# Optimization experiments

Measured on AMD Instinct MI355X. Metric: run time of the kernel, lower is better.

## Reference

```python
import jax, jax.numpy as jnp
import numpy as np

D_STATE = 16


def setup_inputs() -> dict:
    key = jax.random.key(0)
    ks = jax.random.split(key, 7)
    B, S, D = 8, 4096, 64
    ds = D_STATE
    x = jax.random.normal(ks[0], (B, S, D), dtype=jnp.float32)
    # Selection layers modeled as Linear(d_model, out). W_A scaled small so the
    # random transition matrices are contractive over 4096 steps.
    W_A = jax.random.normal(ks[1], (D, ds * ds), dtype=jnp.float32) * 0.01
    b_A = jnp.zeros((ds * ds,), dtype=jnp.float32)
    W_B = jax.random.normal(ks[2], (D, ds * D), dtype=jnp.float32) * 0.05
    b_B = jnp.zeros((ds * D,), dtype=jnp.float32)
    W_C = jax.random.normal(ks[3], (D, ds * D), dtype=jnp.float32) * 0.05
    b_C = jnp.zeros((ds * D,), dtype=jnp.float32)
    return {"x": x, "W_A": W_A, "b_A": b_A, "W_B": W_B, "b_B": b_B,
            "W_C": W_C, "b_C": b_C}


def reference(x, W_A, b_A, W_B, b_B, W_C, b_C):
    B, S, D = x.shape
    ds = D_STATE
    # Input-dependent (selective) parameters per timestep
    A = (x @ W_A + b_A).reshape(B, S, ds, ds)      # [B,S,ds,ds]
    Bm = (x @ W_B + b_B).reshape(B, S, ds, D)      # [B,S,ds,D]
    Cm = (x @ W_C + b_C).reshape(B, S, ds, D)      # [B,S,ds,D]
    # Pre-contract B_t @ x_t once: [B,S,ds]
    Bx = jnp.einsum('bsnd,bsd->bsn', Bm, x)

    def step(h, inputs):
        A_t, Bx_t = inputs                          # [B,ds,ds], [B,ds]
        h = jnp.einsum('bij,bj->bi', A_t, h) + Bx_t
        return h, h

    h0 = jnp.zeros((B, ds), dtype=x.dtype)
    _, hs = jax.lax.scan(step, h0,
                         (jnp.swapaxes(A, 0, 1), jnp.swapaxes(Bx, 0, 1)))
    hs = jnp.swapaxes(hs, 0, 1)                     # [B,S,ds]
    # output_t = C_t^T @ h_t  -> [B,S,D]
    return jnp.einsum('bsnd,bsn->bsd', Cm, hs)
```

## Files before the change

kernel.cpp:

```cpp
#include <hip/hip_runtime.h>

#define BATCH   8
#define SEQ     4096
#define DM      64
#define DS      16
#define BS      (BATCH*SEQ)
#define CHUNK   16
#define NCHT    (BS/CHUNK)
#define SG      16
#define NSG     (NCHT/SG)

typedef __attribute__((ext_vector_type(8))) __bf16 bf16x8;
typedef __attribute__((ext_vector_type(4))) float  f32x4;

__device__ __forceinline__ unsigned short f2bf(float f) {
  unsigned int u = __float_as_uint(f);
  u += 0x7fffu + ((u >> 16) & 1u);
  return (unsigned short)(u >> 16);
}
__device__ __forceinline__ float bflo(unsigned int u) { return __uint_as_float(u << 16); }
__device__ __forceinline__ float bfhi(unsigned int u) { return __uint_as_float(u & 0xffff0000u); }

#define AS_I 20
#define AS_T 324

__global__ __launch_bounds__(256) void k0_castw(
    const float* __restrict__ WA, const float* __restrict__ WB,
    const float* __restrict__ WC,
    unsigned short* __restrict__ WBApk, unsigned short* __restrict__ WCpk)
{
  const int o = blockIdx.x * 256 + threadIdx.x;
  if (o < 81920) {
    int idx = o;
    const int e = idx & 7;    idx >>= 3;
    const int f = idx % 10;   idx /= 10;
    const int quad = idx & 3; idx >>= 2;
    const int l15 = idx & 15; idx >>= 4;
    const int n = idx;
    float src;
    if (f < 8) {
      const int r = f >> 1, h = f & 1;
      src = WB[(h * 32 + quad * 8 + e) * 1024 + (n * 4 + r) * 16 + l15];
    } else {
      const int h = f - 8;
      src = WA[(h * 32 + quad * 8 + e) * 256 + n * 16 + l15];
    }
    WBApk[o] = f2bf(src);
  } else {
    const int p = o - 81920;
    const int e = p & 7;
    const int h = (p >> 3) & 1;
    const int quad = (p >> 4) & 3;
    const int l15 = (p >> 6) & 15;
    const int nr = p >> 10;
    WCpk[p] = f2bf(WC[(h * 32 + quad * 8 + e) * 1024 + nr * 16 + l15]);
  }
}

struct WFrag {
  bf16x8 b00, b01, b10, b11, b20, b21, b30, b31;
  bf16x8 a0f, a1f;
  float  ba;
};

__device__ __forceinline__ WFrag loadw(
    const unsigned short* __restrict__ WBApk,
    const float* __restrict__ bA, int n, int l15, int quad)
{
  WFrag f;
  const bf16x8* fp = (const bf16x8*)(WBApk + (size_t)((n * 16 + l15) * 4 + quad) * 80);
  f.b00 = fp[0]; f.b01 = fp[1];
  f.b10 = fp[2]; f.b11 = fp[3];
  f.b20 = fp[4]; f.b21 = fp[5];
  f.b30 = fp[6]; f.b31 = fp[7];
  f.a0f = fp[8]; f.a1f = fp[9];
  f.ba  = bA[n * 16 + l15];
  return f;
}

__global__ __launch_bounds__(256, 2) void g1(
    const float* __restrict__ x, const unsigned short* __restrict__ WBApk,
    const float* __restrict__ bB,
    const float* __restrict__ bA, unsigned short* __restrict__ xb,
    unsigned short* __restrict__ Wt_ws, float* __restrict__ u_ws,
    float* __restrict__ P_ws, float* __restrict__ v_ws)
{
  __shared__ __align__(16) float xs[64][68];
  __shared__ __align__(16) float bBs[1024];
  __shared__ __align__(16) unsigned short As[64 * AS_T];
  __shared__ __align__(16) float bxs[64][16];
  __shared__ __align__(16) float us[4][16];

  const int tid  = threadIdx.x;
  const int lane = tid & 63;
  const int l15  = lane & 15;
  const int quad = lane >> 4;
  const int w    = tid >> 6;
  const int t0   = blockIdx.x * 64;
  const int twl  = w * 16;

  {
    const float4* xg = (const float4*)(x + (size_t)t0 * DM);
    #pragma unroll
    for (int i = 0; i < 4; ++i) {
      const int f4 = tid + 256 * i;
      ((float4*)&xs[f4 >> 4][0])[f4 & 15] = xg[f4];
    }
    ((float4*)bBs)[tid] = ((const float4*)bB)[tid];
    if (tid < 64) us[tid >> 4][tid & 15] = 0.f;
  }
  __syncthreads();

  WFrag cur = loadw(WBApk, bA, 0, l15, quad);

  bf16x8 a0, a1;
  {
    const int row = twl + l15;
    union { bf16x8 v; ushort4 s[2]; } ua, ub;
    float4 p0 = *(const float4*)&xs[row][quad * 8];
    float4 p1 = *(const float4*)&xs[row][quad * 8 + 4];
    float4 p2 = *(const float4*)&xs[row][32 + quad * 8];
    float4 p3 = *(const float4*)&xs[row][32 + quad * 8 + 4];
    ua.s[0] = (ushort4){f2bf(p0.x), f2bf(p0.y), f2bf(p0.z), f2bf(p0.w)};
    ua.s[1] = (ushort4){f2bf(p1.x), f2bf(p1.y), f2bf(p1.z), f2bf(p1.w)};
    ub.s[0] = (ushort4){f2bf(p2.x), f2bf(p2.y), f2bf(p2.z), f2bf(p2.w)};
    ub.s[1] = (ushort4){f2bf(p3.x), f2bf(p3.y), f2bf(p3.z), f2bf(p3.w)};
    a0 = ua.v; a1 = ub.v;
    unsigned short* xp = xb + (size_t)(t0 + row) * 64 + quad * 8;
    *(bf16x8*)xp        = a0;
    *(bf16x8*)(xp + 32) = a1;
  }

  float xv[4][4];
  #pragma unroll
  for (int r = 0; r < 4; ++r)
    #pragma unroll
    for (int reg = 0; reg < 4; ++reg)
      xv[r][reg] = xs[twl + quad * 4 + reg][r * 16 + l15];

  #pragma unroll
  for (int n = 0; n < 16; ++n) {
    WFrag nxt = (n < 15) ? loadw(WBApk, bA, n + 1, l15, quad) : cur;

    const f32x4 z4 = {0.f, 0.f, 0.f, 0.f};
    f32x4 aac = z4;
    aac = __builtin_amdgcn_mfma_f32_16x16x32_bf16(a0, cur.a0f, aac, 0, 0, 0);
    aac = __builtin_amdgcn_mfma_f32_16x16x32_bf16(a1, cur.a1f, aac, 0, 0, 0);

    f32x4 ac0 = z4, ac1 = z4, ac2 = z4, ac3 = z4;
    ac0 = __builtin_amdgcn_mfma_f32_16x16x32_bf16(a0, cur.b00, ac0, 0, 0, 0);
    ac0 = __builtin_amdgcn_mfma_f32_16x16x32_bf16(a1, cur.b01, ac0, 0, 0, 0);
    ac1 = __builtin_amdgcn_mfma_f32_16x16x32_bf16(a0, cur.b10, ac1, 0, 0, 0);
    ac1 = __builtin_amdgcn_mfma_f32_16x16x32_bf16(a1, cur.b11, ac1, 0, 0, 0);
    ac2 = __builtin_amdgcn_mfma_f32_16x16x32_bf16(a0, cur.b20, ac2, 0, 0, 0);
    ac2 = __builtin_amdgcn_mfma_f32_16x16x32_bf16(a1, cur.b21, ac2, 0, 0, 0);
    ac3 = __builtin_amdgcn_mfma_f32_16x16x32_bf16(a0, cur.b30, ac3, 0, 0, 0);
    ac3 = __builtin_amdgcn_mfma_f32_16x16x32_bf16(a1, cur.b31, ac3, 0, 0, 0);

    const float bb0 = bBs[n * 64 +  0 + l15];
    const float bb1 = bBs[n * 64 + 16 + l15];
    const float bb2 = bBs[n * 64 + 32 + l15];
    const float bb3 = bBs[n * 64 + 48 + l15];
    float part[4];
    #pragma unroll
    for (int reg = 0; reg < 4; ++reg) {
      float s = fmaf(ac0[reg] + bb0, xv[0][reg], 0.f);
      s = fmaf(ac1[reg] + bb1, xv[1][reg], s);
      s = fmaf(ac2[reg] + bb2, xv[2][reg], s);
      s = fmaf(ac3[reg] + bb3, xv[3][reg], s);
      part[reg] = s;
    }
    #pragma unroll
    for (int off = 1; off < 16; off <<= 1) {
      #pragma unroll
      for (int reg = 0; reg < 4; ++reg)
        part[reg] += __shfl_xor(part[reg], off, 64);
    }
    if (l15 == 0) {
      #pragma unroll
      for (int reg = 0; reg < 4; ++reg)
        bxs[twl + quad * 4 + reg][n] = part[reg];
    }

    As[(twl + quad * 4 + 0) * AS_T + n * AS_I + l15] = f2bf(aac[0] + cur.ba);
    As[(twl + quad * 4 + 1) * AS_T + n * AS_I + l15] = f2bf(aac[1] + cur.ba);
    As[(twl + quad * 4 + 2) * AS_T + n * AS_I + l15] = f2bf(aac[2] + cur.ba);
    As[(twl + quad * 4 + 3) * AS_T + n * AS_I + l15] = f2bf(aac[3] + cur.ba);

    cur = nxt;
  }

  {
    bf16x8 wb;
    #pragma unroll
    for (int j = 0; j < 8; ++j) wb[j] = (__bf16)((quad * 8 + j == l15) ? 1.f : 0.f);
    f32x4 d = {0.f, 0.f, 0.f, 0.f};
    const int qq = quad & 1;

    const unsigned short* rpp = &As[twl * AS_T + l15 * AS_I];
    uint2 r0 = *(const uint2*)(rpp);
    uint2 r1 = *(const uint2*)(rpp + 4);
    uint2 r2 = *(const uint2*)(rpp + 8);
    uint2 r3 = *(const uint2*)(rpp + 12);

    #pragma unroll 1
    for (int t = 0; t < CHUNK; ++t) {
      const int tl = twl + t;

      uint2 s0, s1, s2, s3;
      if (t < CHUNK - 1) {
        const unsigned short* rp = &As[(tl + 1) * AS_T + l15 * AS_I];
        s0 = *(const uint2*)(rp);
        s1 = *(const uint2*)(rp + 4);
        s2 = *(const uint2*)(rp + 8);
        s3 = *(const uint2*)(rp + 12);
      } else { s0 = r0; s1 = r1; s2 = r2; s3 = r3; }

      uint4 abits;
      if (quad == 0)      abits = make_uint4(r0.x, r0.y, r1.x, r1.y);
      else if (quad == 1) abits = make_uint4(r2.x, r2.y, r3.x, r3.y);
      else                abits = make_uint4(0u, 0u, 0u, 0u);
      bf16x8 af = *(bf16x8*)&abits;

      f32x4 z4 = {0.f, 0.f, 0.f, 0.f};
      d = __builtin_amdgcn_mfma_f32_16x16x32_bf16(af, wb, z4, 0, 0, 0);

      float nu;
      {
        float4 U0 = *(const float4*)&us[w][0];
        float4 U1 = *(const float4*)&us[w][4];
        float4 U2 = *(const float4*)&us[w][8];
        float4 U3 = *(const float4*)&us[w][12];
        float n0 = bxs[tl][l15], n1 = 0.f, n2 = 0.f, n3 = 0.f;
        n0 = fmaf(bflo(r0.x), U0.x, n0); n0 = fmaf(bfhi(r0.x), U0.y, n0);
        n0 = fmaf(bflo(r0.y), U0.z, n0); n0 = fmaf(bfhi(r0.y), U0.w, n0);
        n1 = fmaf(bflo(r1.x), U1.x, n1); n1 = fmaf(bfhi(r1.x), U1.y, n1);
        n1 = fmaf(bflo(r1.y), U1.z, n1); n1 = fmaf(bfhi(r1.y), U1.w, n1);
        n2 = fmaf(bflo(r2.x), U2.x, n2); n2 = fmaf(bfhi(r2.x), U2.y, n2);
        n2 = fmaf(bflo(r2.y), U2.z, n2); n2 = fmaf(bfhi(r2.y), U2.w, n2);
        n3 = fmaf(bflo(r3.x), U3.x, n3); n3 = fmaf(bfhi(r3.x), U3.y, n3);
        n3 = fmaf(bflo(r3.y), U3.z, n3); n3 = fmaf(bfhi(r3.y), U3.w, n3);
        nu = (n0 + n1) + (n2 + n3);
      }

      bf16x8 nb;
      nb[0] = (__bf16)__shfl(d[0], (2 * qq + 0) * 16 + l15, 64);
      nb[1] = (__bf16)__shfl(d[1], (2 * qq + 0) * 16 + l15, 64);
      nb[2] = (__bf16)__shfl(d[2], (2 * qq + 0) * 16 + l15, 64);
      nb[3] = (__bf16)__shfl(d[3], (2 * qq + 0) * 16 + l15, 64);
      nb[4] = (__bf16)__shfl(d[0], (2 * qq + 1) * 16 + l15, 64);
      nb[5] = (__bf16)__shfl(d[1], (2 * qq + 1) * 16 + l15, 64);
      nb[6] = (__bf16)__shfl(d[2], (2 * qq + 1) * 16 + l15, 64);
      nb[7] = (__bf16)__shfl(d[3], (2 * qq + 1) * 16 + l15, 64);
      wb = nb;

      if (quad == 0) {
        us[w][l15] = nu;
        bxs[tl][l15] = nu;
      }
      #pragma unroll
      for (int r = 0; r < 4; ++r)
        As[tl * AS_T + (quad * 4 + r) * AS_I + l15] = f2bf(d[r]);

      r0 = s0; r1 = s1; r2 = s2; r3 = s3;
    }

    const int chunk = blockIdx.x * 4 + w;
    #pragma unroll
    for (int r = 0; r < 4; ++r)
      P_ws[(size_t)chunk * 256 + (quad * 4 + r) * 16 + l15] = d[r];
    if (quad == 0) v_ws[(size_t)chunk * DS + l15] = us[w][l15];
  }
  __syncthreads();

  {
    uint4* Wg = (uint4*)(Wt_ws + (size_t)t0 * 256);
    #pragma unroll 1
    for (int z = 0; z < 8; ++z) {
      const int p4 = z * 256 + tid;
      const int f  = p4 * 8;
      const int t  = f >> 8, i = (f >> 4) & 15, k = f & 15;
      const unsigned short* sp = &As[t * AS_T + i * AS_I + k];
      uint2 lo = *(const uint2*)(sp);
      uint2 hi = *(const uint2*)(sp + 4);
      Wg[p4] = make_uint4(lo.x, lo.y, hi.x, hi.y);
    }
    ((float4*)(u_ws + (size_t)t0 * DS))[tid] = ((const float4*)&bxs[0][0])[tid];
  }
}

__global__ __launch_bounds__(1024, 4) void k3f(
    const float* __restrict__ P_ws, const float* __restrict__ v_ws,
    float* __restrict__ hb_ws,
    const unsigned short* __restrict__ Wt_ws,
    const unsigned short* __restrict__ xb,
    const float* __restrict__ u_ws)
{
  __shared__ float Qs[16][256];
  __shared__ float wsv[16][16];
  __shared__ float hbgs[16][16];

  const int tid = threadIdx.x;
  const int bx  = blockIdx.x;

  if (bx >= 8) {
    const uint4* wp = (const uint4*)(Wt_ws + (size_t)bx * 32 * 256);
    uint4 a = wp[tid];
    const unsigned int* xp = (const unsigned int*)(xb + (size_t)bx * 32 * 64);
    unsigned int b = xp[tid];
    unsigned int c = 0;
    if (tid < 512) c = ((const unsigned int*)(u_ws + (size_t)bx * 32 * DS))[tid];
    asm volatile("" :: "v"(a.x), "v"(b), "v"(c));
    return;
  }

  const int lane = tid & 63;
  const int l15  = lane & 15;
  const int quad = lane >> 4;
  const int wv   = tid >> 6;
  const int qq   = quad & 1;

  {
    const int s = bx * 16 + wv;
    if (lane < 16) wsv[wv][lane] = 0.f;
    bf16x8 wb;
    #pragma unroll
    for (int j = 0; j < 8; ++j) wb[j] = (__bf16)((quad * 8 + j == l15) ? 1.f : 0.f);
    f32x4 d = {0.f, 0.f, 0.f, 0.f};

    float4 p0 = {0.f,0.f,0.f,0.f}, p1 = {0.f,0.f,0.f,0.f};
    float nv;
    {
      const int chunk = s * SG;
      if (quad < 2) {
        const float4* pr = (const float4*)(P_ws + (size_t)chunk * 256 + l15 * 16 + quad * 8);
        p0 = pr[0]; p1 = pr[1];
      }
      nv = v_ws[(size_t)chunk * DS + l15];
    }

    #pragma unroll 1
    for (int t = 0; t < SG; ++t) {
      float4 q0 = {0.f,0.f,0.f,0.f}, q1 = {0.f,0.f,0.f,0.f};
      float nv2 = 0.f;
      if (t < SG - 1) {
        const int chunk = s * SG + t + 1;
        if (quad < 2) {
          const float4* pr = (const float4*)(P_ws + (size_t)chunk * 256 + l15 * 16 + quad * 8);
          q0 = pr[0]; q1 = pr[1];
        }
        nv2 = v_ws[(size_t)chunk * DS + l15];
      }

      bf16x8 af;
      af[0] = (__bf16)p0.x; af[1] = (__bf16)p0.y; af[2] = (__bf16)p0.z; af[3] = (__bf16)p0.w;
      af[4] = (__bf16)p1.x; af[5] = (__bf16)p1.y; af[6] = (__bf16)p1.z; af[7] = (__bf16)p1.w;

      f32x4 z4 = {0.f, 0.f, 0.f, 0.f};
      d = __builtin_amdgcn_mfma_f32_16x16x32_bf16(af, wb, z4, 0, 0, 0);

      float part = 0.f;
      if (quad < 2) {
        const float* wrow = &wsv[wv][quad * 8];
        part = p0.x*wrow[0] + p0.y*wrow[1] + p0.z*wrow[2] + p0.w*wrow[3]
             + p1.x*wrow[4] + p1.y*wrow[5] + p1.z*wrow[6] + p1.w*wrow[7];
      }
      part += __shfl_xor(part, 16, 64);

      bf16x8 nb;
      nb[0] = (__bf16)__shfl(d[0], (2 * qq + 0) * 16 + l15, 64);
      nb[1] = (__bf16)__shfl(d[1], (2 * qq + 0) * 16 + l15, 64);
      nb[2] = (__bf16)__shfl(d[2], (2 * qq + 0) * 16 + l15, 64);
      nb[3] = (__bf16)__shfl(d[3], (2 * qq + 0) * 16 + l15, 64);
      nb[4] = (__bf16)__shfl(d[0], (2 * qq + 1) * 16 + l15, 64);
      nb[5] = (__bf16)__shfl(d[1], (2 * qq + 1) * 16 + l15, 64);
      nb[6] = (__bf16)__shfl(d[2], (2 * qq + 1) * 16 + l15, 64);
      nb[7] = (__bf16)__shfl(d[3], (2 * qq + 1) * 16 + l15, 64);
      wb = nb;

      if (quad == 0) wsv[wv][l15] = part + nv;

      p0 = q0; p1 = q1; nv = nv2;
    }

    #pragma unroll
    for (int r = 0; r < 4; ++r)
      Qs[wv][(quad * 4 + r) * 16 + l15] = d[r];
  }
  __syncthreads();

  if (tid < 16) {
    const int r = tid;
    float h = 0.f;
    #pragma unroll 1
    for (int g = 0; g < 16; ++g) {
      hbgs[g][r] = h;
      const float4* Pr = (const float4*)&Qs[g][r * 16];
      float4 c0 = Pr[0], c1 = Pr[1], c2 = Pr[2], c3 = Pr[3];
      const float vc = wsv[g][r];
      float a0 = c0.x*__shfl(h, 0,16) + c0.y*__shfl(h, 1,16) + c0.z*__shfl(h, 2,16) + c0.w*__shfl(h, 3,16);
      float a1 = c1.x*__shfl(h, 4,16) + c1.y*__shfl(h, 5,16) + c1.z*__shfl(h, 6,16) + c1.w*__shfl(h, 7,16);
      float a2 = c2.x*__shfl(h, 8,16) + c2.y*__shfl(h, 9,16) + c2.z*__shfl(h,10,16) + c2.w*__shfl(h,11,16);
      float a3 = c3.x*__shfl(h,12,16) + c3.y*__shfl(h,13,16) + c3.z*__shfl(h,14,16) + c3.w*__shfl(h,15,16);
      h = vc + ((a0 + a1) + (a2 + a3));
    }
  }
  __syncthreads();

  if (tid < 256) {
    const int g = tid >> 4;
    const int r = tid & 15;
    const int s = bx * 16 + g;
    float h = hbgs[g][r];

    float4 c0, c1, c2, c3; float vc;
    {
      const int chunk = s * SG;
      const float4* Pr = (const float4*)&P_ws[(size_t)chunk * 256 + r * 16];
      c0 = Pr[0]; c1 = Pr[1]; c2 = Pr[2]; c3 = Pr[3];
      vc = v_ws[(size_t)chunk * DS + r];
    }

    #pragma unroll 1
    for (int t = 0; t < SG; ++t) {
      const int chunk = s * SG + t;
      float4 d0, d1, d2, d3; float vc2;
      if (t < SG - 1) {
        const float4* Pr = (const float4*)&P_ws[(size_t)(chunk + 1) * 256 + r * 16];
        d0 = Pr[0]; d1 = Pr[1]; d2 = Pr[2]; d3 = Pr[3];
        vc2 = v_ws[(size_t)(chunk + 1) * DS + r];
      } else { d0 = c0; d1 = c1; d2 = c2; d3 = c3; vc2 = vc; }

      hb_ws[(size_t)chunk * DS + r] = h;
      float a0 = c0.x*__shfl(h, 0,16) + c0.y*__shfl(h, 1,16) + c0.z*__shfl(h, 2,16) + c0.w*__shfl(h, 3,16);
      float a1 = c1.x*__shfl(h, 4,16) + c1.y*__shfl(h, 5,16) + c1.z*__shfl(h, 6,16) + c1.w*__shfl(h, 7,16);
      float a2 = c2.x*__shfl(h, 8,16) + c2.y*__shfl(h, 9,16) + c2.z*__shfl(h,10,16) + c2.w*__shfl(h,11,16);
      float a3 = c3.x*__shfl(h,12,16) + c3.y*__shfl(h,13,16) + c3.z*__shfl(h,14,16) + c3.w*__shfl(h,15,16);
      h = vc + ((a0 + a1) + (a2 + a3));

      c0 = d0; c1 = d1; c2 = d2; c3 = d3; vc = vc2;
    }
  }
}

struct CFrag2 {
  bf16x8 c00, c01, c10, c11;
};

__device__ __forceinline__ CFrag2 loadc2(
    const unsigned short* __restrict__ WCpk, int n, int r0c, int r1c, int l15, int quad)
{
  CFrag2 f;
  const bf16x8* p0 = (const bf16x8*)(WCpk + (size_t)((n * 4 + r0c) * 64 + l15 * 4 + quad) * 16);
  const bf16x8* p1 = (const bf16x8*)(WCpk + (size_t)((n * 4 + r1c) * 64 + l15 * 4 + quad) * 16);
  f.c00 = p0[0]; f.c01 = p0[1];
  f.c10 = p1[0]; f.c11 = p1[1];
  return f;
}

__global__ __launch_bounds__(256, 4) void g2(
    const unsigned short* __restrict__ xb, const unsigned short* __restrict__ WCpk,
    const float* __restrict__ bC, const unsigned short* __restrict__ Wt_ws,
    const float* __restrict__ u_ws, const float* __restrict__ hb_ws,
    float* __restrict__ out)
{
  __shared__ float hsh[32][17];
  __shared__ float bCs[1024];
  const int tid  = threadIdx.x;
  const int lane = tid & 63;
  const int l15  = lane & 15;
  const int quad = lane >> 4;
  const int w    = tid >> 6;
  const int tg   = w >> 1;
  const int dh   = w & 1;
  const int t0   = blockIdx.x * 32;
  const int twl  = tg * 16;
  const int r0c  = dh * 2 + 0;
  const int r1c  = dh * 2 + 1;

  ((float4*)bCs)[tid] = ((const float4*)bC)[tid];

  const bf16x8* xvp = (const bf16x8*)(xb + (size_t)(t0 + twl + l15) * 64);
  bf16x8 a0 = xvp[quad];
  bf16x8 a1 = xvp[quad + 4];

  #pragma unroll
  for (int z = 0; z < 2; ++z) {
    const int gcell = z * 256 + tid;
    const int tl = gcell >> 4, i = gcell & 15;
    const int t = t0 + tl;
    const uint4* wr = (const uint4*)(Wt_ws + (size_t)t * 256 + i * 16);
    uint4 wa = wr[0], wbv = wr[1];
    const float4* hp = (const float4*)(hb_ws + (size_t)(t >> 4) * DS);
    float4 h0 = hp[0], h1 = hp[1], h2 = hp[2], h3 = hp[3];
    float p0 = u_ws[(size_t)t * DS + i], p1 = 0.f, p2 = 0.f, p3 = 0.f;
    p0 = fmaf(bflo(wa.x),  h0.x, p0); p0 = fmaf(bfhi(wa.x),  h0.y, p0);
    p0 = fmaf(bflo(wa.y),  h0.z, p0); p0 = fmaf(bfhi(wa.y),  h0.w, p0);
    p1 = fmaf(bflo(wa.z),  h1.x, p1); p1 = fmaf(bfhi(wa.z),  h1.y, p1);
    p1 = fmaf(bflo(wa.w),  h1.z, p1); p1 = fmaf(bfhi(wa.w),  h1.w, p1);
    p2 = fmaf(bflo(wbv.x), h2.x, p2); p2 = fmaf(bfhi(wbv.x), h2.y, p2);
    p2 = fmaf(bflo(wbv.y), h2.z, p2); p2 = fmaf(bfhi(wbv.y), h2.w, p2);
    p3 = fmaf(bflo(wbv.z), h3.x, p3); p3 = fmaf(bfhi(wbv.z), h3.y, p3);
    p3 = fmaf(bflo(wbv.w), h3.z, p3); p3 = fmaf(bfhi(wbv.w), h3.w, p3);
    hsh[tl][i] = (p0 + p1) + (p2 + p3);
  }
  __syncthreads();

  f32x4 o0 = {0.f, 0.f, 0.f, 0.f}, o1 = {0.f, 0.f, 0.f, 0.f};

  CFrag2 cur = loadc2(WCpk, 0, r0c, r1c, l15, quad);
  #pragma unroll
  for (int n = 0; n < 16; ++n) {
    CFrag2 nxt = (n < 15) ? loadc2(WCpk, n + 1, r0c, r1c, l15, quad) : cur;

    const f32x4 z4 = {0.f, 0.f, 0.f, 0.f};
    f32x4 ac0 = z4, ac1 = z4;
    ac0 = __builtin_amdgcn_mfma_f32_16x16x32_bf16(a0, cur.c00, ac0, 0, 0, 0);
    ac0 = __builtin_amdgcn_mfma_f32_16x16x32_bf16(a1, cur.c01, ac0, 0, 0, 0);
    ac1 = __builtin_amdgcn_mfma_f32_16x16x32_bf16(a0, cur.c10, ac1, 0, 0, 0);
    ac1 = __builtin_amdgcn_mfma_f32_16x16x32_bf16(a1, cur.c11, ac1, 0, 0, 0);

    float hn[4];
    #pragma unroll
    for (int reg = 0; reg < 4; ++reg) hn[reg] = hsh[twl + quad * 4 + reg][n];

    const float bc0 = bCs[n * 64 + r0c * 16 + l15];
    const float bc1 = bCs[n * 64 + r1c * 16 + l15];
    #pragma unroll
    for (int reg = 0; reg < 4; ++reg) {
      o0[reg] = fmaf(ac0[reg] + bc0, hn[reg], o0[reg]);
      o1[reg] = fmaf(ac1[reg] + bc1, hn[reg], o1[reg]);
    }

    cur = nxt;
  }

  #pragma unroll
  for (int reg = 0; reg < 4; ++reg) {
    out[(size_t)(t0 + twl + quad * 4 + reg) * DM + r0c * 16 + l15] = o0[reg];
    out[(size_t)(t0 + twl + quad * 4 + reg) * DM + r1c * 16 + l15] = o1[reg];
  }
}

extern "C" void kernel_launch(void* const* d_in, const int* in_sizes, int n_in,
                              void* d_out, int out_size, void* d_ws, size_t ws_size,
                              hipStream_t stream) {
  const float* x  = (const float*)d_in[0];
  const float* WA = (const float*)d_in[1];
  const float* bA = (const float*)d_in[2];
  const float* WB = (const float*)d_in[3];
  const float* bB = (const float*)d_in[4];
  const float* WC = (const float*)d_in[5];
  const float* bC = (const float*)d_in[6];
  float* out = (float*)d_out;

  float* ws     = (float*)d_ws;
  float* P_ws   = ws;
  float* v_ws   = P_ws   + (size_t)NCHT * 256;
  float* u_ws   = v_ws   + (size_t)NCHT * DS;
  float* Q_ws   = u_ws   + (size_t)BS * DS;
  float* w_ws   = Q_ws   + (size_t)NSG * 256;
  float* hbg_ws = w_ws   + (size_t)NSG * DS;
  float* hb_ws  = hbg_ws + (size_t)NSG * DS;
  unsigned short* xb    = (unsigned short*)(hb_ws + (size_t)NCHT * DS);
  unsigned short* WBApk = xb    + (size_t)BS * 64;
  unsigned short* WCpk  = WBApk + 81920;
  unsigned short* Wt_ws = WCpk  + 65536;

  k0_castw<<<576,      256, 0, stream>>>(WA, WB, WC, WBApk, WCpk);
  g1      <<<BS / 64,  256, 0, stream>>>(x, WBApk, bB, bA, xb, Wt_ws, u_ws, P_ws, v_ws);
  k3f     <<<1024,    1024, 0, stream>>>(P_ws, v_ws, hb_ws, Wt_ws, xb, u_ws);
  g2      <<<BS / 32,  256, 0, stream>>>(xb, WCpk, bC, Wt_ws, u_ws, hb_ws, out);
}
```

Baseline: 182.6 us.

## Split g1 into projection kernel and chunk-scan kernel with halved per-wave work

```diff
diff --git a/kernel.cpp b/kernel.cpp
--- a/kernel.cpp
+++ b/kernel.cpp
@@ -78,40 +78,40 @@
   return f;
 }
 
-__global__ __launch_bounds__(256, 2) void g1(
+__global__ __launch_bounds__(256, 4) void g1a(
     const float* __restrict__ x, const unsigned short* __restrict__ WBApk,
-    const float* __restrict__ bB,
-    const float* __restrict__ bA, unsigned short* __restrict__ xb,
-    unsigned short* __restrict__ Wt_ws, float* __restrict__ u_ws,
-    float* __restrict__ P_ws, float* __restrict__ v_ws)
+    const float* __restrict__ bB, const float* __restrict__ bA,
+    unsigned short* __restrict__ xb, unsigned short* __restrict__ Wt_ws,
+    float* __restrict__ u_ws)
 {
-  __shared__ __align__(16) float xs[64][68];
+  __shared__ __align__(16) float xs[32][68];
   __shared__ __align__(16) float bBs[1024];
-  __shared__ __align__(16) unsigned short As[64 * AS_T];
-  __shared__ __align__(16) float bxs[64][16];
-  __shared__ __align__(16) float us[4][16];
+  __shared__ __align__(16) unsigned short As[32 * AS_T];
+  __shared__ __align__(16) float bxs[32][16];
 
   const int tid  = threadIdx.x;
   const int lane = tid & 63;
   const int l15  = lane & 15;
   const int quad = lane >> 4;
   const int w    = tid >> 6;
-  const int t0   = blockIdx.x * 64;
-  const int twl  = w * 16;
+  const int tg   = w >> 1;
+  const int nh   = w & 1;
+  const int t0   = blockIdx.x * 32;
+  const int twl  = tg * 16;
+  const int n0   = nh * 8;
 
   {
     const float4* xg = (const float4*)(x + (size_t)t0 * DM);
     #pragma unroll
-    for (int i = 0; i < 4; ++i) {
+    for (int i = 0; i < 2; ++i) {
       const int f4 = tid + 256 * i;
       ((float4*)&xs[f4 >> 4][0])[f4 & 15] = xg[f4];
     }
     ((float4*)bBs)[tid] = ((const float4*)bB)[tid];
-    if (tid < 64) us[tid >> 4][tid & 15] = 0.f;
   }
   __syncthreads();
 
-  WFrag cur = loadw(WBApk, bA, 0, l15, quad);
+  WFrag cur = loadw(WBApk, bA, n0, l15, quad);
 
   bf16x8 a0, a1;
   {
@@ -126,9 +126,11 @@
     ub.s[0] = (ushort4){f2bf(p2.x), f2bf(p2.y), f2bf(p2.z), f2bf(p2.w)};
     ub.s[1] = (ushort4){f2bf(p3.x), f2bf(p3.y), f2bf(p3.z), f2bf(p3.w)};
     a0 = ua.v; a1 = ub.v;
-    unsigned short* xp = xb + (size_t)(t0 + row) * 64 + quad * 8;
-    *(bf16x8*)xp        = a0;
-    *(bf16x8*)(xp + 32) = a1;
+    if (nh == 0) {
+      unsigned short* xp = xb + (size_t)(t0 + row) * 64 + quad * 8;
+      *(bf16x8*)xp        = a0;
+      *(bf16x8*)(xp + 32) = a1;
+    }
   }
 
   float xv[4][4];
@@ -139,8 +141,9 @@
       xv[r][reg] = xs[twl + quad * 4 + reg][r * 16 + l15];
 
   #pragma unroll
-  for (int n = 0; n < 16; ++n) {
-    WFrag nxt = (n < 15) ? loadw(WBApk, bA, n + 1, l15, quad) : cur;
+  for (int j = 0; j < 8; ++j) {
+    const int n = n0 + j;
+    WFrag nxt = (j < 7) ? loadw(WBApk, bA, n + 1, l15, quad) : cur;
 
     const f32x4 z4 = {0.f, 0.f, 0.f, 0.f};
     f32x4 aac = z4;
@@ -189,6 +192,57 @@
 
     cur = nxt;
   }
+  __syncthreads();
+
+  {
+    uint4* Wg = (uint4*)(Wt_ws + (size_t)t0 * 256);
+    #pragma unroll 1
+    for (int z = 0; z < 4; ++z) {
+      const int p4 = z * 256 + tid;
+      const int f  = p4 * 8;
+      const int t  = f >> 8, i = (f >> 4) & 15, k = f & 15;
+      const unsigned short* sp = &As[t * AS_T + i * AS_I + k];
+      uint2 lo = *(const uint2*)(sp);
+      uint2 hi = *(const uint2*)(sp + 4);
+      Wg[p4] = make_uint4(lo.x, lo.y, hi.x, hi.y);
+    }
+    if (tid < 128)
+      ((float4*)(u_ws + (size_t)t0 * DS))[tid] = ((const float4*)&bxs[0][0])[tid];
+  }
+}
+
+__global__ __launch_bounds__(256, 2) void g1b(
+    unsigned short* __restrict__ Wt_ws, float* __restrict__ u_ws,
+    float* __restrict__ P_ws, float* __restrict__ v_ws)
+{
+  __shared__ __align__(16) unsigned short As[64 * AS_T];
+  __shared__ __align__(16) float bxs[64][16];
+  __shared__ __align__(16) float us[4][16];
+
+  const int tid  = threadIdx.x;
+  const int lane = tid & 63;
+  const int l15  = lane & 15;
+  const int quad = lane >> 4;
+  const int w    = tid >> 6;
+  const int t0   = blockIdx.x * 64;
+  const int twl  = w * 16;
+
+  {
+    const uint4* Wg = (const uint4*)(Wt_ws + (size_t)t0 * 256);
+    #pragma unroll 1
+    for (int z = 0; z < 8; ++z) {
+      const int p4 = z * 256 + tid;
+      const int f  = p4 * 8;
+      const int t  = f >> 8, i = (f >> 4) & 15, k = f & 15;
+      uint4 v = Wg[p4];
+      unsigned short* sp = &As[t * AS_T + i * AS_I + k];
+      *(uint2*)(sp)     = make_uint2(v.x, v.y);
+      *(uint2*)(sp + 4) = make_uint2(v.z, v.w);
+    }
+    ((float4*)bxs)[tid] = ((const float4*)(u_ws + (size_t)t0 * DS))[tid];
+    if (tid < 64) us[tid >> 4][tid & 15] = 0.f;
+  }
+  __syncthreads();
 
   {
     bf16x8 wb;
@@ -568,7 +622,8 @@
   unsigned short* Wt_ws = WCpk  + 65536;
 
   k0_castw<<<576,      256, 0, stream>>>(WA, WB, WC, WBApk, WCpk);
-  g1      <<<BS / 64,  256, 0, stream>>>(x, WBApk, bB, bA, xb, Wt_ws, u_ws, P_ws, v_ws);
+  g1a     <<<BS / 32,  256, 0, stream>>>(x, WBApk, bB, bA, xb, Wt_ws, u_ws);
+  g1b     <<<BS / 64,  256, 0, stream>>>(Wt_ws, u_ws, P_ws, v_ws);
   k3f     <<<1024,    1024, 0, stream>>>(P_ws, v_ws, hb_ws, Wt_ws, xb, u_ws);
   g2      <<<BS / 32,  256, 0, stream>>>(xb, WCpk, bC, Wt_ws, u_ws, hb_ws, out);
 }
```

Result: slower. 191.3 us (+4.8%).
